# Kernel tuning notes

Hardware: AMD Instinct MI355X
Metric: run time of the kernel (lower is better)

Reference implementation:

```python
import jax, jax.numpy as jnp
import numpy as np

EPS_RMS = 1.1920929e-07  # torch.finfo(float32).eps, RMSNorm default when eps=None
EPS_BN = 1e-5            # BatchNorm1d default eps
NUM_CODES = 4096
EMBED_DIM = 64


def rms_norm(x):
    # nn.RMSNorm(embed_dim, elementwise_affine=False)
    ms = jnp.mean(x * x, axis=-1, keepdims=True)
    return x * jax.lax.rsqrt(ms + EPS_RMS)


def get_codebook(codebook_weight, bn_weight, bn_bias):
    # BatchNorm1d with track_running_stats=False: batch stats over codebook rows
    mean = jnp.mean(codebook_weight, axis=0)
    var = jnp.var(codebook_weight, axis=0)  # biased variance, as torch BN uses
    h = (codebook_weight - mean) * jax.lax.rsqrt(var + EPS_BN) * bn_weight + bn_bias
    return rms_norm(h)


def setup_inputs() -> dict:
    key = jax.random.key(0)
    k1, k2 = jax.random.split(key)
    z = jax.random.normal(k1, (8, 4096, EMBED_DIM), dtype=jnp.float32)
    # codebook init: uniform(-1/num_codes, 1/num_codes)
    codebook_weight = jax.random.uniform(
        k2, (NUM_CODES, EMBED_DIM), dtype=jnp.float32,
        minval=-1.0 / NUM_CODES, maxval=1.0 / NUM_CODES)
    bn_weight = jnp.ones((EMBED_DIM,), dtype=jnp.float32)
    bn_bias = jnp.zeros((EMBED_DIM,), dtype=jnp.float32)
    return {"z": z, "codebook_weight": codebook_weight,
            "bn_weight": bn_weight, "bn_bias": bn_bias}


def reference(z, codebook_weight, bn_weight, bn_bias):
    # c_in / c_out are Identity since width == embed_dim
    z_e = rms_norm(z)                                   # [B, S, D]
    cb = get_codebook(codebook_weight, bn_weight, bn_bias)  # [K, D]

    z_flat = z_e.reshape(-1, z_e.shape[-1])             # [N, D]
    # argmin of cdist == argmin of squared distance (sqrt is monotone)
    d2 = (jnp.sum(z_flat * z_flat, axis=1, keepdims=True)
          - 2.0 * (z_flat @ cb.T)
          + jnp.sum(cb * cb, axis=1))                   # [N, K]
    q = jnp.argmin(d2, axis=1)                          # [N]

    z_q = cb[q].reshape(z_e.shape)                      # gather codes
    q = q.reshape(z_e.shape[:-1])

    # straight-through: gradient flows to z_e only
    z_q_st = z_e + jax.lax.stop_gradient(z_q - z_e)
    # ret_dict entries: 'z' (detached z_e), 'q', 'z_q' (detached)
    return (z_q_st, jax.lax.stop_gradient(z_e), q, jax.lax.stop_gradient(z_q))
```

## Files before the change

### kernel.cpp

```cpp
#include <hip/hip_runtime.h>
#include <math.h>

#define NROWS 32768
#define DIM   64
#define NCODE 4096
#define EPS_RMS 1.1920929e-07f
#define EPS_BN  1e-5f

typedef _Float16 f16x8 __attribute__((ext_vector_type(8)));
typedef float    f32x4 __attribute__((ext_vector_type(4)));

#define WS_PS   0
#define WS_PQ   16384
#define WS_CC   32768
#define WS_CB32 49152
#define WS_PH   (49152 + 1048576)
#define WS_PL   (WS_PH + 524288)

#define OUT1 ((size_t)NROWS * DIM)
#define OUT2 ((size_t)2 * NROWS * DIM)
#define OUT3 (OUT2 + NROWS)

#define MFMA16(a, b, c) __builtin_amdgcn_mfma_f32_16x16x32_f16(a, b, c, 0, 0, 0)

__device__ __forceinline__ void gload16(void* lds, const void* g) {
    __builtin_amdgcn_global_load_lds(
        (const __attribute__((address_space(1))) unsigned int*)g,
        (__attribute__((address_space(3))) unsigned int*)lds, 16, 0, 0);
}

__global__ __launch_bounds__(256) void k_bn1(const float* __restrict__ w,
                                             char* __restrict__ wsb) {
    __shared__ float s1[4][64], s2[4][64];
    int lane = threadIdx.x & 63, v = threadIdx.x >> 6;
    long base = (long)blockIdx.x * 64 + v * 16;
    float s = 0.f, sq = 0.f;
    #pragma unroll
    for (int i = 0; i < 16; i++) {
        float x = w[(base + i) * DIM + lane];
        s += x; sq += x * x;
    }
    s1[v][lane] = s; s2[v][lane] = sq;
    __syncthreads();
    if (threadIdx.x < 64) {
        float ts = s1[0][lane] + s1[1][lane] + s1[2][lane] + s1[3][lane];
        float tq = s2[0][lane] + s2[1][lane] + s2[2][lane] + s2[3][lane];
        ((float*)(wsb + WS_PS))[blockIdx.x * 64 + lane] = ts;
        ((float*)(wsb + WS_PQ))[blockIdx.x * 64 + lane] = tq;
    }
}

__global__ __launch_bounds__(256) void k_cb(const float* __restrict__ w,
                                            const float* __restrict__ bnw,
                                            const float* __restrict__ bnb,
                                            char* __restrict__ wsb) {
    __shared__ float s1[4][64], s2[4][64], af[64], bf[64];
    __shared__ _Float16 sh[16][64], sl[16][64];
    int t = threadIdx.x, lane = t & 63, v = t >> 6;
    const float* ps = (const float*)(wsb + WS_PS);
    const float* pq = (const float*)(wsb + WS_PQ);
    float s = 0.f, sq = 0.f;
    #pragma unroll
    for (int b = 0; b < 16; b++) {
        s  += ps[(v * 16 + b) * 64 + lane];
        sq += pq[(v * 16 + b) * 64 + lane];
    }
    s1[v][lane] = s; s2[v][lane] = sq;
    __syncthreads();
    if (t < 64) {
        float ts = s1[0][lane] + s1[1][lane] + s1[2][lane] + s1[3][lane];
        float tq = s2[0][lane] + s2[1][lane] + s2[2][lane] + s2[3][lane];
        float mean = ts * (1.0f / NCODE);
        float var  = tq * (1.0f / NCODE) - mean * mean;
        float a = rsqrtf(var + EPS_BN) * bnw[lane];
        af[lane] = a;
        bf[lane] = bnb[lane] - mean * a;
    }
    __syncthreads();
    float a = af[lane], bb = bf[lane];
    float* cb32 = (float*)(wsb + WS_CB32);
    float* ccp  = (float*)(wsb + WS_CC);
    int g = blockIdx.x;
    #pragma unroll
    for (int i = 0; i < 4; i++) {
        int  rl  = v * 4 + i;
        long row = (long)g * 16 + rl;
        float x = w[row * DIM + lane];
        float h = fmaf(x, a, bb);
        float ss = h * h;
        #pragma unroll
        for (int m = 1; m < 64; m <<= 1) ss += __shfl_xor(ss, m);
        float rms = rsqrtf(ss * (1.0f / DIM) + EPS_RMS);
        float c = h * rms;
        cb32[row * DIM + lane] = c;
        _Float16 ch = (_Float16)c;
        sh[rl][lane] = ch;
        sl[rl][lane] = (_Float16)(c - (float)ch);
        float cs = c * c;
        #pragma unroll
        for (int m = 1; m < 64; m <<= 1) cs += __shfl_xor(cs, m);
        if (lane == 0) ccp[row] = -0.5f * cs;
    }
    __syncthreads();
    {
        int u = t & 127;
        int c = u >> 6, l = u & 63;
        int codel = l & 15;
        int kbase = c * 32 + (l >> 4) * 8;
        size_t dst = (size_t)((g * 2 + c) * 64 + l) * 16;
        if (t < 128) {
            *(f16x8*)(wsb + WS_PH + dst) = *(const f16x8*)&sh[codel][kbase];
        } else {
            *(f16x8*)(wsb + WS_PL + dst) = *(const f16x8*)&sl[codel][kbase];
        }
    }
}

__global__ __launch_bounds__(512, 2) void k_main(const float* __restrict__ z,
                                                 char* __restrict__ wsb,
                                                 float* __restrict__ out) {
    __shared__ __align__(16) unsigned char sm[98304];

    const int tid  = threadIdx.x;
    const int lane = tid & 63;
    const int w    = tid >> 6;
    const int rg   = w & 3;
    const int ch   = w >> 2;
    const int l15  = lane & 15;
    const int l4   = lane >> 4;
    const long rowbase = (long)blockIdx.x * 128;

    const float* ccnG = (const float*)(wsb + WS_CC);
    const float* cb32 = (const float*)(wsb + WS_CB32);

    const char* pH = wsb + WS_PH + w * 1024 + lane * 16;
    const char* pL = wsb + WS_PL + w * 1024 + lane * 16;

    #define STAGE(p, bufoff)                                                \
    {                                                                       \
        const char* gh = pH + (size_t)(p) * 16384;                          \
        const char* gl = pL + (size_t)(p) * 16384;                          \
        gload16(sm + (bufoff) + w * 1024,          gh);                     \
        gload16(sm + (bufoff) + 8192 + w * 1024,   gh + 8192);              \
        gload16(sm + (bufoff) + 16384 + w * 1024,  gl);                     \
        gload16(sm + (bufoff) + 24576 + w * 1024,  gl + 8192);              \
    }

    STAGE(0, 0);

    {
        int r = tid >> 2, seg = tid & 3;
        const float4* zp = (const float4*)(z + (rowbase + r) * DIM + seg * 16);
        float4 v4[4];
        float ss = 0.f;
        #pragma unroll
        for (int i = 0; i < 4; i++) {
            v4[i] = zp[i];
            ss += v4[i].x * v4[i].x + v4[i].y * v4[i].y + v4[i].z * v4[i].z + v4[i].w * v4[i].w;
        }
        ss += __shfl_xor(ss, 1);
        ss += __shfl_xor(ss, 2);
        float rms = rsqrtf(ss * (1.0f / DIM) + EPS_RMS);
        float4* oz = (float4*)(out + OUT1 + (rowbase + r) * DIM + seg * 16);
        __align__(16) _Float16 hb[16], lb[16];
        #pragma unroll
        for (int i = 0; i < 4; i++) {
            float xs[4] = {v4[i].x, v4[i].y, v4[i].z, v4[i].w};
            #pragma unroll
            for (int j = 0; j < 4; j++) {
                float x = xs[j] * rms;
                _Float16 h = (_Float16)x;
                hb[i * 4 + j] = h;
                lb[i * 4 + j] = (_Float16)(x - (float)h);
                xs[j] = x;
            }
            oz[i] = make_float4(xs[0], xs[1], xs[2], xs[3]);
        }
        unsigned char* zhp = sm + 65536 + r * 128 + seg * 32;
        ((f16x8*)zhp)[0] = ((f16x8*)hb)[0];
        ((f16x8*)zhp)[1] = ((f16x8*)hb)[1];
        unsigned char* zlp = zhp + 16384;
        ((f16x8*)zlp)[0] = ((f16x8*)lb)[0];
        ((f16x8*)zlp)[1] = ((f16x8*)lb)[1];
    }
    __syncthreads();

    f16x8 ah[2][2], al[2][2];
    #pragma unroll
    for (int s = 0; s < 2; s++)
        #pragma unroll
        for (int c = 0; c < 2; c++) {
            int off = 65536 + (rg * 32 + s * 16 + l15) * 128 + c * 64 + l4 * 16;
            ah[s][c] = *(const f16x8*)(sm + off);
            al[s][c] = *(const f16x8*)(sm + 16384 + off);
        }

    float bmax[2][4];
    int   bix[2][4];
    #pragma unroll
    for (int s = 0; s < 2; s++)
        #pragma unroll
        for (int r = 0; r < 4; r++) { bmax[s][r] = -3.4e38f; bix[s][r] = 0; }

    float ccv[4];
    #pragma unroll
    for (int q = 0; q < 4; q++)
        ccv[q] = ccnG[ch * 64 + q * 16 + l15];

    #define COMPUTE(p, bufoff)                                                     \
    {                                                                              \
        _Pragma("unroll")                                                          \
        for (int q = 0; q < 4; q++) {                                              \
            f16x8 bh[2], bl[2];                                                    \
            _Pragma("unroll")                                                      \
            for (int c = 0; c < 2; c++) {                                          \
                int boff = (bufoff) + (ch * 8 + q * 2 + c) * 1024 + lane * 16;     \
                bh[c] = *(const f16x8*)(sm + boff);                                \
                bl[c] = *(const f16x8*)(sm + 16384 + boff);                        \
            }                                                                      \
            int code = (p) * 128 + ch * 64 + q * 16 + l15;                         \
            _Pragma("unroll")                                                      \
            for (int s = 0; s < 2; s++) {                                          \
                f32x4 a2 = {ccv[q], ccv[q], ccv[q], ccv[q]};                       \
                a2 = MFMA16(ah[s][0], bh[0], a2);                                  \
                a2 = MFMA16(ah[s][1], bh[1], a2);                                  \
                a2 = MFMA16(ah[s][0], bl[0], a2);                                  \
                a2 = MFMA16(ah[s][1], bl[1], a2);                                  \
                a2 = MFMA16(al[s][0], bh[0], a2);                                  \
                a2 = MFMA16(al[s][1], bh[1], a2);                                  \
                _Pragma("unroll")                                                  \
                for (int r = 0; r < 4; r++) {                                      \
                    if (a2[r] > bmax[s][r]) { bmax[s][r] = a2[r]; bix[s][r] = code; } \
                }                                                                  \
            }                                                                      \
        }                                                                          \
    }

    #pragma unroll 1
    for (int p = 0; p < 31; ++p) {
        STAGE(p + 1, ((p + 1) & 1) * 32768);
        float ccn_nx[4];
        {
            const float* cn = ccnG + (p + 1) * 128 + ch * 64 + l15;
            #pragma unroll
            for (int q = 0; q < 4; q++) ccn_nx[q] = cn[q * 16];
        }

        COMPUTE(p, (p & 1) * 32768);

        __syncthreads();
        #pragma unroll
        for (int q = 0; q < 4; q++) ccv[q] = ccn_nx[q];
    }
    COMPUTE(31, 32768);

    float* redd = (float*)sm;
    int*   redi = (int*)(sm + 1024);
    int*   bidx = (int*)(sm + 2048);
    #pragma unroll
    for (int s = 0; s < 2; s++)
        #pragma unroll
        for (int r = 0; r < 4; r++) {
            float d = bmax[s][r];
            int   ix = bix[s][r];
            #pragma unroll
            for (int m = 1; m < 16; m <<= 1) {
                float od = __shfl_xor(d, m);
                int   oi = __shfl_xor(ix, m);
                if (od > d || (od == d && oi < ix)) { d = od; ix = oi; }
            }
            if (l15 == 0) {
                int row = rg * 32 + s * 16 + l4 * 4 + r;
                redd[row * 2 + ch] = d;
                redi[row * 2 + ch] = ix;
            }
        }
    __syncthreads();
    if (tid < 128) {
        float d0 = redd[tid * 2 + 0];
        int   i0 = redi[tid * 2 + 0];
        float d1 = redd[tid * 2 + 1];
        int   i1 = redi[tid * 2 + 1];
        float bv = d0; int bi_ = i0;
        if (d1 > bv || (d1 == bv && i1 < bi_)) { bv = d1; bi_ = i1; }
        bidx[tid] = bi_;
        out[OUT2 + rowbase + tid] = (float)bi_;
    }
    __syncthreads();
    {
        int r = tid >> 2, seg = tid & 3;
        int ix = bidx[r];
        const float4* src = (const float4*)(cb32 + (long)ix * DIM + seg * 16);
        float4* o0 = (float4*)(out + (rowbase + r) * DIM + seg * 16);
        float4* o3 = (float4*)(out + OUT3 + (rowbase + r) * DIM + seg * 16);
        #pragma unroll
        for (int i = 0; i < 4; i++) { float4 t4 = src[i]; o0[i] = t4; o3[i] = t4; }
    }
}

extern "C" void kernel_launch(void* const* d_in, const int* in_sizes, int n_in,
                              void* d_out, int out_size, void* d_ws, size_t ws_size,
                              hipStream_t stream) {
    const float* z   = (const float*)d_in[0];
    const float* w   = (const float*)d_in[1];
    const float* bnw = (const float*)d_in[2];
    const float* bnb = (const float*)d_in[3];
    float* out = (float*)d_out;
    char*  wsb = (char*)d_ws;

    k_bn1 <<<64,  256, 0, stream>>>(w, wsb);
    k_cb  <<<256, 256, 0, stream>>>(w, bnw, bnb, wsb);
    k_main<<<256, 512, 0, stream>>>(z, wsb, out);
}
```

Measured before the change: 75.88 us.

## Replace double-buffered codebook staging with 4-deep LDS ring and manual waitcnt

```diff
diff --git a/kernel.cpp b/kernel.cpp
--- a/kernel.cpp
+++ b/kernel.cpp
@@ -119,34 +119,34 @@
 __global__ __launch_bounds__(512, 2) void k_main(const float* __restrict__ z,
                                                  char* __restrict__ wsb,
                                                  float* __restrict__ out) {
-    __shared__ __align__(16) unsigned char sm[98304];
+    __shared__ __align__(16) unsigned char sm[114688];
 
     const int tid  = threadIdx.x;
     const int lane = tid & 63;
     const int w    = tid >> 6;
-    const int rg   = w & 3;
-    const int ch   = w >> 2;
+    const int rg   = w >> 1;
+    const int ch   = w & 1;
     const int l15  = lane & 15;
     const int l4   = lane >> 4;
     const long rowbase = (long)blockIdx.x * 128;
 
-    const float* ccnG = (const float*)(wsb + WS_CC);
     const float* cb32 = (const float*)(wsb + WS_CB32);
 
-    const char* pH = wsb + WS_PH + w * 1024 + lane * 16;
-    const char* pL = wsb + WS_PL + w * 1024 + lane * 16;
-
-    #define STAGE(p, bufoff)                                                \
-    {                                                                       \
-        const char* gh = pH + (size_t)(p) * 16384;                          \
-        const char* gl = pL + (size_t)(p) * 16384;                          \
-        gload16(sm + (bufoff) + w * 1024,          gh);                     \
-        gload16(sm + (bufoff) + 8192 + w * 1024,   gh + 8192);              \
-        gload16(sm + (bufoff) + 16384 + w * 1024,  gl);                     \
-        gload16(sm + (bufoff) + 24576 + w * 1024,  gl + 8192);              \
-    }
-
-    STAGE(0, 0);
+    #define RING(t) (((t) & 3) * 16384)
+    #define STAGE(t)                                                              \
+    {                                                                             \
+        const char* gh_ = wsb + WS_PH + (size_t)(t) * 8192 + (w * 1024 + lane * 16); \
+        const char* gl_ = wsb + WS_PL + (size_t)(t) * 8192 + (w * 1024 + lane * 16); \
+        gload16(sm + RING(t) + w * 1024,        gh_);                             \
+        gload16(sm + RING(t) + 8192 + w * 1024, gl_);                             \
+    }
+
+    STAGE(0); STAGE(1); STAGE(2);
+    {
+        const char* gc = wsb + WS_CC + (w * 1024 + lane * 16);
+        gload16(sm + 98304 + w * 1024, gc);
+        gload16(sm + 98304 + 8192 + w * 1024, gc + 8192);
+    }
 
     {
         int r = tid >> 2, seg = tid & 3;
@@ -202,57 +202,52 @@
         #pragma unroll
         for (int r = 0; r < 4; r++) { bmax[s][r] = -3.4e38f; bix[s][r] = 0; }
 
-    float ccv[4];
-    #pragma unroll
-    for (int q = 0; q < 4; q++)
-        ccv[q] = ccnG[ch * 64 + q * 16 + l15];
-
-    #define COMPUTE(p, bufoff)                                                     \
-    {                                                                              \
-        _Pragma("unroll")                                                          \
-        for (int q = 0; q < 4; q++) {                                              \
-            f16x8 bh[2], bl[2];                                                    \
-            _Pragma("unroll")                                                      \
-            for (int c = 0; c < 2; c++) {                                          \
-                int boff = (bufoff) + (ch * 8 + q * 2 + c) * 1024 + lane * 16;     \
-                bh[c] = *(const f16x8*)(sm + boff);                                \
-                bl[c] = *(const f16x8*)(sm + 16384 + boff);                        \
-            }                                                                      \
-            int code = (p) * 128 + ch * 64 + q * 16 + l15;                         \
-            _Pragma("unroll")                                                      \
-            for (int s = 0; s < 2; s++) {                                          \
-                f32x4 a2 = {ccv[q], ccv[q], ccv[q], ccv[q]};                       \
-                a2 = MFMA16(ah[s][0], bh[0], a2);                                  \
-                a2 = MFMA16(ah[s][1], bh[1], a2);                                  \
-                a2 = MFMA16(ah[s][0], bl[0], a2);                                  \
-                a2 = MFMA16(ah[s][1], bl[1], a2);                                  \
-                a2 = MFMA16(al[s][0], bh[0], a2);                                  \
-                a2 = MFMA16(al[s][1], bh[1], a2);                                  \
-                _Pragma("unroll")                                                  \
-                for (int r = 0; r < 4; r++) {                                      \
-                    if (a2[r] > bmax[s][r]) { bmax[s][r] = a2[r]; bix[s][r] = code; } \
-                }                                                                  \
-            }                                                                      \
-        }                                                                          \
-    }
-
     #pragma unroll 1
-    for (int p = 0; p < 31; ++p) {
-        STAGE(p + 1, ((p + 1) & 1) * 32768);
-        float ccn_nx[4];
-        {
-            const float* cn = ccnG + (p + 1) * 128 + ch * 64 + l15;
+    for (int t = 0; t < 64; ++t) {
+        if (t + 3 < 64) STAGE(t + 3);
+
+        const unsigned char* buf = sm + RING(t);
+        float ccv[2];
+        ccv[0] = *(const float*)(sm + 98304 + (size_t)(t * 64 + ch * 32 + l15) * 4);
+        ccv[1] = *(const float*)(sm + 98304 + (size_t)(t * 64 + ch * 32 + 16 + l15) * 4);
+
+        f16x8 bh[2][2], bl[2][2];
+        #pragma unroll
+        for (int q = 0; q < 2; q++)
             #pragma unroll
-            for (int q = 0; q < 4; q++) ccn_nx[q] = cn[q * 16];
-        }
-
-        COMPUTE(p, (p & 1) * 32768);
-
-        __syncthreads();
-        #pragma unroll
-        for (int q = 0; q < 4; q++) ccv[q] = ccn_nx[q];
-    }
-    COMPUTE(31, 32768);
+            for (int c = 0; c < 2; c++) {
+                int gl_ = (ch * 2 + q) * 2 + c;
+                bh[q][c] = *(const f16x8*)(buf + gl_ * 1024 + lane * 16);
+                bl[q][c] = *(const f16x8*)(buf + 8192 + gl_ * 1024 + lane * 16);
+            }
+
+        __builtin_amdgcn_s_setprio(1);
+        #pragma unroll
+        for (int q = 0; q < 2; q++) {
+            int code = t * 64 + ch * 32 + q * 16 + l15;
+            #pragma unroll
+            for (int s = 0; s < 2; s++) {
+                f32x4 a2 = {ccv[q], ccv[q], ccv[q], ccv[q]};
+                a2 = MFMA16(ah[s][0], bh[q][0], a2);
+                a2 = MFMA16(ah[s][1], bh[q][1], a2);
+                a2 = MFMA16(ah[s][0], bl[q][0], a2);
+                a2 = MFMA16(ah[s][1], bl[q][1], a2);
+                a2 = MFMA16(al[s][0], bh[q][0], a2);
+                a2 = MFMA16(al[s][1], bh[q][1], a2);
+                #pragma unroll
+                for (int r = 0; r < 4; r++) {
+                    if (a2[r] > bmax[s][r]) { bmax[s][r] = a2[r]; bix[s][r] = code; }
+                }
+            }
+        }
+        __builtin_amdgcn_s_setprio(0);
+
+        asm volatile("s_waitcnt vmcnt(4)" ::: "memory");
+        asm volatile("s_barrier" ::: "memory");
+        __builtin_amdgcn_sched_barrier(0);
+    }
+
+    __syncthreads();
 
     float* redd = (float*)sm;
     int*   redi = (int*)(sm + 1024);
```

After: 74.94 us. No clear change (-1.2%).
